# Kernel tuning notes

Hardware: AMD Instinct MI355X
Metric: run time of the kernel (lower is better)

The kernel has to match this reference:

```python
import jax, jax.numpy as jnp
import numpy as np

B, N, L, D, V = 32, 2048, 128, 1024, 32000

def setup_inputs() -> dict:
    key = jax.random.key(0)
    k1, k2, k3 = jax.random.split(key, 3)
    image_features = jax.random.normal(k1, (B, N, D), dtype=jnp.float32)
    token_ids = jax.random.randint(k2, (B, L), 0, V, dtype=jnp.int64)
    emb_table = jax.random.normal(k3, (V, D), dtype=jnp.float32)
    return {"image_features": image_features, "token_ids": token_ids, "emb_table": emb_table}

def reference(image_features, token_ids, emb_table):
    # targets = embeddings(input_ids): [B, L, D]
    targets = emb_table[token_ids]
    # batched pairwise L2 distance (torch.cdist p=2): ||x-y|| via the
    # expanded form ||x||^2 + ||y||^2 - 2<x,y>, clamped for numerical safety.
    x2 = jnp.sum(image_features * image_features, axis=-1)        # [B, N]
    y2 = jnp.sum(targets * targets, axis=-1)                      # [B, L]
    xy = jnp.einsum('bnd,bld->bnl', image_features, targets)      # [B, N, L]
    d2 = x2[:, :, None] + y2[:, None, :] - 2.0 * xy
    costs = jnp.sqrt(jnp.maximum(d2, 0.0))                        # [B, N, L]
    smallest = jnp.min(costs, axis=-1)                            # [B, N]
    return smallest.mean()
```

## Files before the change

kernel.cpp:

```cpp
#include <hip/hip_runtime.h>
#include <cstdint>
#include <cstddef>

#define BATCH 32
#define NROW  2048
#define LTOK  128
#define DDIM  1024

#define BM    128
#define BK    64
#define LDST  72

typedef short s8v  __attribute__((ext_vector_type(8)));
typedef float f4v  __attribute__((ext_vector_type(4)));

__device__ __forceinline__ uint32_t pk2(float lo, float hi) {
    return __builtin_amdgcn_perm(__float_as_uint(hi), __float_as_uint(lo), 0x07060302u);
}

__global__ __launch_bounds__(256)
void prep_y(const int*   __restrict__ tok,
            const float* __restrict__ E,
            uint32_t*    __restrict__ Ybf,
            float*       __restrict__ y2)
{
    const int l = blockIdx.x, b = blockIdx.y;
    const int tid = threadIdx.x;
    const int t = tok[b * LTOK + l];
    const float4 v = ((const float4*)(E + (size_t)t * DDIM))[tid];
    float s = v.x*v.x + v.y*v.y + v.z*v.z + v.w*v.w;
    uint2 p; p.x = pk2(v.x, v.y); p.y = pk2(v.z, v.w);
    ((uint2*)(Ybf + ((size_t)(b * LTOK + l) * DDIM) / 2))[tid] = p;
#pragma unroll
    for (int o = 1; o < 64; o <<= 1) s += __shfl_xor(s, o);
    __shared__ float ws4[4];
    if ((tid & 63) == 0) ws4[tid >> 6] = s;
    __syncthreads();
    if (tid == 0) y2[b * LTOK + l] = ws4[0] + ws4[1] + ws4[2] + ws4[3];
}

__global__ __launch_bounds__(256, 2)
void cdist_min_mean_kernel(const float* __restrict__ X,
                           const short* __restrict__ Ybf,
                           const float* __restrict__ y2g,
                           float* __restrict__ out)
{
    __shared__ __align__(16) short Xs[BM * LDST];
    __shared__ __align__(16) short Ys[LTOK * 64];
    __shared__ float x2s[BM];
    __shared__ float rowmin[BM * 2];
    __shared__ float wsum[4];

    const int tid  = threadIdx.x;
    const int lane = tid & 63;
    const int wid  = tid >> 6;
    const int grp  = tid >> 3;
    const int sub  = tid & 7;

    const int b       = blockIdx.y;
    const int rowBase = blockIdx.x * BM;

    const float* Xg = X + ((size_t)b * NROW + rowBase) * DDIM;

    const float* xp[4];
#pragma unroll
    for (int i = 0; i < 4; ++i)
        xp[i] = Xg + (size_t)(grp + 32 * i) * DDIM + sub * 8;

    const short* yg[4];
#pragma unroll
    for (int it = 0; it < 4; ++it) {
        int c   = it * 256 + tid;
        int row = c >> 3;
        int chs = (c & 7) ^ (row & 7);
        yg[it] = Ybf + (size_t)(b * LTOK + row) * DDIM + chs * 8;
    }

    f4v acc[4][4];
#pragma unroll
    for (int mi = 0; mi < 4; ++mi)
#pragma unroll
        for (int ni = 0; ni < 4; ++ni)
            acc[mi][ni] = (f4v){0.f, 0.f, 0.f, 0.f};

    float xacc[4] = {0.f, 0.f, 0.f, 0.f};

    const int quad = lane >> 4;
    const int l15  = lane & 15;
    const int wm   = wid >> 1;
    const int wn   = wid & 1;

    for (int k0 = 0; k0 < DDIM; k0 += BK) {
        float4 xa[4], xb[4];
#pragma unroll
        for (int i = 0; i < 4; ++i) {
            xa[i] = *(const float4*)(xp[i] + k0);
            xb[i] = *(const float4*)(xp[i] + k0 + 4);
        }
        __syncthreads();

#pragma unroll
        for (int it = 0; it < 4; ++it)
            __builtin_amdgcn_global_load_lds(
                (const __attribute__((address_space(1))) void*)(yg[it] + k0),
                (__attribute__((address_space(3))) void*)&Ys[(it * 256 + (wid << 6)) * 8],
                16, 0, 0);

#pragma unroll
        for (int i = 0; i < 4; ++i) {
            const float4 a = xa[i], c4 = xb[i];
            xacc[i] += a.x*a.x + a.y*a.y + a.z*a.z + a.w*a.w
                     + c4.x*c4.x + c4.y*c4.y + c4.z*c4.z + c4.w*c4.w;
            uint4 p;
            p.x = pk2(a.x, a.y);  p.y = pk2(a.z, a.w);
            p.z = pk2(c4.x, c4.y); p.w = pk2(c4.z, c4.w);
            *(uint4*)&Xs[(grp + 32 * i) * LDST + sub * 8] = p;
        }
        __syncthreads();

#pragma unroll
        for (int ks = 0; ks < BK; ks += 32) {
            s8v af[4], bfr[4];
#pragma unroll
            for (int mi = 0; mi < 4; ++mi)
                af[mi] = *(const s8v*)&Xs[(wm * 64 + mi * 16 + l15) * LDST + ks + quad * 8];
#pragma unroll
            for (int ni = 0; ni < 4; ++ni) {
                int brow = wn * 64 + ni * 16 + l15;
                int ch   = ((ks >> 3) + quad) ^ (brow & 7);
                bfr[ni]  = *(const s8v*)&Ys[brow * 64 + ch * 8];
            }
#pragma unroll
            for (int mi = 0; mi < 4; ++mi)
#pragma unroll
                for (int ni = 0; ni < 4; ++ni)
                    acc[mi][ni] = __builtin_amdgcn_mfma_f32_16x16x32_bf16(
                        af[mi], bfr[ni], acc[mi][ni], 0, 0, 0);
        }
    }

#pragma unroll
    for (int i = 0; i < 4; ++i) {
        float s = xacc[i];
        s += __shfl_xor(s, 1); s += __shfl_xor(s, 2); s += __shfl_xor(s, 4);
        if ((lane & 7) == 0) x2s[grp + 32 * i] = s;
    }
    __syncthreads();

    float y2r[4];
#pragma unroll
    for (int ni = 0; ni < 4; ++ni)
        y2r[ni] = y2g[b * LTOK + wn * 64 + ni * 16 + l15];

#pragma unroll
    for (int mi = 0; mi < 4; ++mi) {
#pragma unroll
        for (int j = 0; j < 4; ++j) {
            float m = y2r[0] - 2.f * acc[mi][0][j];
            m = fminf(m, y2r[1] - 2.f * acc[mi][1][j]);
            m = fminf(m, y2r[2] - 2.f * acc[mi][2][j]);
            m = fminf(m, y2r[3] - 2.f * acc[mi][3][j]);
            m = fminf(m, __shfl_xor(m, 1));
            m = fminf(m, __shfl_xor(m, 2));
            m = fminf(m, __shfl_xor(m, 4));
            m = fminf(m, __shfl_xor(m, 8));
            if (l15 == 0)
                rowmin[(wm * 64 + mi * 16 + quad * 4 + j) * 2 + wn] = m;
        }
    }
    __syncthreads();

    float part = 0.f;
    if (tid < BM) {
        float m = fminf(rowmin[tid * 2], rowmin[tid * 2 + 1]);
        part = sqrtf(fmaxf(x2s[tid] + m, 0.f));
    }
#pragma unroll
    for (int s = 1; s < 64; s <<= 1) part += __shfl_xor(part, s);
    if (lane == 0) wsum[wid] = part;
    __syncthreads();
    if (tid == 0) {
        float tot = (wsum[0] + wsum[1] + wsum[2] + wsum[3])
                  * (1.0f / (float)(BATCH * NROW));
        atomicAdd(out, tot);
    }
}

extern "C" void kernel_launch(void* const* d_in, const int* in_sizes, int n_in,
                              void* d_out, int out_size, void* d_ws, size_t ws_size,
                              hipStream_t stream) {
    const float* X   = (const float*)d_in[0];
    const int*   tok = (const int*)d_in[1];
    const float* E   = (const float*)d_in[2];
    float* out = (float*)d_out;

    uint32_t* Ybf = (uint32_t*)d_ws;
    float*    y2  = (float*)((char*)d_ws + (size_t)BATCH * LTOK * DDIM * 2);

    hipMemsetAsync(out, 0, sizeof(float), stream);

    dim3 pgrid(LTOK, BATCH, 1);
    prep_y<<<pgrid, 256, 0, stream>>>(tok, E, Ybf, y2);

    dim3 grid(NROW / BM, BATCH, 1);
    cdist_min_mean_kernel<<<grid, 256, 0, stream>>>(X, (const short*)Ybf, y2, out);
}
```

Baseline: 440.1 us.

## Drop LDS staging; feed MFMA fragments straight from global with prepacked Y

```diff
diff --git a/kernel.cpp b/kernel.cpp
--- a/kernel.cpp
+++ b/kernel.cpp
@@ -6,13 +6,11 @@
 #define NROW  2048
 #define LTOK  128
 #define DDIM  1024
+#define BM    64
+#define KC    (DDIM / 8)
 
-#define BM    128
-#define BK    64
-#define LDST  72
-
-typedef short s8v  __attribute__((ext_vector_type(8)));
-typedef float f4v  __attribute__((ext_vector_type(4)));
+typedef short s8v __attribute__((ext_vector_type(8)));
+typedef float f4v __attribute__((ext_vector_type(4)));
 
 __device__ __forceinline__ uint32_t pk2(float lo, float hi) {
     return __builtin_amdgcn_perm(__float_as_uint(hi), __float_as_uint(lo), 0x07060302u);
@@ -21,32 +19,30 @@
 __global__ __launch_bounds__(256)
 void prep_y(const int*   __restrict__ tok,
             const float* __restrict__ E,
-            uint32_t*    __restrict__ Ybf,
+            uint32_t*    __restrict__ Ypk,
             float*       __restrict__ y2)
 {
-    const int l = blockIdx.x, b = blockIdx.y;
-    const int tid = threadIdx.x;
-    const int t = tok[b * LTOK + l];
-    const float4 v = ((const float4*)(E + (size_t)t * DDIM))[tid];
+    const int t = blockIdx.x, b = blockIdx.y, tid = threadIdx.x;
+    const int tr = tok[b * LTOK + t];
+    const float4 v = ((const float4*)(E + (size_t)tr * DDIM))[tid];
     float s = v.x*v.x + v.y*v.y + v.z*v.z + v.w*v.w;
+    const int kc = tid >> 1;
     uint2 p; p.x = pk2(v.x, v.y); p.y = pk2(v.z, v.w);
-    ((uint2*)(Ybf + ((size_t)(b * LTOK + l) * DDIM) / 2))[tid] = p;
+    *(uint2*)(Ypk + (((size_t)(b * KC + kc) * LTOK + t) << 2) + ((tid & 1) << 1)) = p;
 #pragma unroll
     for (int o = 1; o < 64; o <<= 1) s += __shfl_xor(s, o);
     __shared__ float ws4[4];
     if ((tid & 63) == 0) ws4[tid >> 6] = s;
     __syncthreads();
-    if (tid == 0) y2[b * LTOK + l] = ws4[0] + ws4[1] + ws4[2] + ws4[3];
+    if (tid == 0) y2[b * LTOK + t] = ws4[0] + ws4[1] + ws4[2] + ws4[3];
 }
 
-__global__ __launch_bounds__(256, 2)
+__global__ __launch_bounds__(256, 4)
 void cdist_min_mean_kernel(const float* __restrict__ X,
-                           const short* __restrict__ Ybf,
+                           const short* __restrict__ Ypk,
                            const float* __restrict__ y2g,
                            float* __restrict__ out)
 {
-    __shared__ __align__(16) short Xs[BM * LDST];
-    __shared__ __align__(16) short Ys[LTOK * 64];
     __shared__ float x2s[BM];
     __shared__ float rowmin[BM * 2];
     __shared__ float wsum[4];
@@ -54,106 +50,88 @@
     const int tid  = threadIdx.x;
     const int lane = tid & 63;
     const int wid  = tid >> 6;
-    const int grp  = tid >> 3;
-    const int sub  = tid & 7;
+    const int l15  = lane & 15;
+    const int quad = lane >> 4;
+    const int wrow = wid >> 1;
+    const int wcol = wid & 1;
 
-    const int b       = blockIdx.y;
-    const int rowBase = blockIdx.x * BM;
+    const int L   = blockIdx.x;
+    const int xcd = L & 7;
+    const int s   = L >> 3;
+    const int b   = (xcd << 2) | (s >> 5);
+    const int rowBase = (s & 31) * BM;
 
-    const float* Xg = X + ((size_t)b * NROW + rowBase) * DDIM;
-
-    const float* xp[4];
+    const float* xp[2];
 #pragma unroll
-    for (int i = 0; i < 4; ++i)
-        xp[i] = Xg + (size_t)(grp + 32 * i) * DDIM + sub * 8;
-
-    const short* yg[4];
+    for (int mi = 0; mi < 2; ++mi) {
+        int row = rowBase + wrow * 32 + mi * 16 + l15;
+        xp[mi] = X + ((size_t)b * NROW + row) * DDIM + quad * 8;
+    }
+    const s8v* ypp[4];
 #pragma unroll
-    for (int it = 0; it < 4; ++it) {
-        int c   = it * 256 + tid;
-        int row = c >> 3;
-        int chs = (c & 7) ^ (row & 7);
-        yg[it] = Ybf + (size_t)(b * LTOK + row) * DDIM + chs * 8;
+    for (int ni = 0; ni < 4; ++ni) {
+        int tcol = wcol * 64 + ni * 16 + l15;
+        ypp[ni] = (const s8v*)Ypk + ((size_t)(b * KC + quad) * LTOK + tcol);
     }
 
-    f4v acc[4][4];
+    f4v acc[2][4];
 #pragma unroll
-    for (int mi = 0; mi < 4; ++mi)
+    for (int mi = 0; mi < 2; ++mi)
 #pragma unroll
         for (int ni = 0; ni < 4; ++ni)
             acc[mi][ni] = (f4v){0.f, 0.f, 0.f, 0.f};
 
-    float xacc[4] = {0.f, 0.f, 0.f, 0.f};
+    float xs2[2] = {0.f, 0.f};
 
-    const int quad = lane >> 4;
-    const int l15  = lane & 15;
-    const int wm   = wid >> 1;
-    const int wn   = wid & 1;
+#pragma unroll 2
+    for (int k0 = 0; k0 < DDIM; k0 += 32) {
+        float4 xa[2], xb[2];
+#pragma unroll
+        for (int mi = 0; mi < 2; ++mi) {
+            xa[mi] = *(const float4*)(xp[mi] + k0);
+            xb[mi] = *(const float4*)(xp[mi] + k0 + 4);
+        }
+        s8v bfr[4];
+        const int yoff = (k0 >> 3) * LTOK;
+#pragma unroll
+        for (int ni = 0; ni < 4; ++ni)
+            bfr[ni] = ypp[ni][yoff];
 
-    for (int k0 = 0; k0 < DDIM; k0 += BK) {
-        float4 xa[4], xb[4];
+        s8v afr[2];
 #pragma unroll
-        for (int i = 0; i < 4; ++i) {
-            xa[i] = *(const float4*)(xp[i] + k0);
-            xb[i] = *(const float4*)(xp[i] + k0 + 4);
+        for (int mi = 0; mi < 2; ++mi) {
+            const float4 a = xa[mi], c = xb[mi];
+            if (wcol == 0)
+                xs2[mi] += a.x*a.x + a.y*a.y + a.z*a.z + a.w*a.w
+                         + c.x*c.x + c.y*c.y + c.z*c.z + c.w*c.w;
+            uint4 p;
+            p.x = pk2(a.x, a.y); p.y = pk2(a.z, a.w);
+            p.z = pk2(c.x, c.y); p.w = pk2(c.z, c.w);
+            afr[mi] = *(s8v*)&p;
         }
-        __syncthreads();
-
 #pragma unroll
-        for (int it = 0; it < 4; ++it)
-            __builtin_amdgcn_global_load_lds(
-                (const __attribute__((address_space(1))) void*)(yg[it] + k0),
-                (__attribute__((address_space(3))) void*)&Ys[(it * 256 + (wid << 6)) * 8],
-                16, 0, 0);
-
+        for (int mi = 0; mi < 2; ++mi)
 #pragma unroll
-        for (int i = 0; i < 4; ++i) {
-            const float4 a = xa[i], c4 = xb[i];
-            xacc[i] += a.x*a.x + a.y*a.y + a.z*a.z + a.w*a.w
-                     + c4.x*c4.x + c4.y*c4.y + c4.z*c4.z + c4.w*c4.w;
-            uint4 p;
-            p.x = pk2(a.x, a.y);  p.y = pk2(a.z, a.w);
-            p.z = pk2(c4.x, c4.y); p.w = pk2(c4.z, c4.w);
-            *(uint4*)&Xs[(grp + 32 * i) * LDST + sub * 8] = p;
-        }
-        __syncthreads();
-
-#pragma unroll
-        for (int ks = 0; ks < BK; ks += 32) {
-            s8v af[4], bfr[4];
-#pragma unroll
-            for (int mi = 0; mi < 4; ++mi)
-                af[mi] = *(const s8v*)&Xs[(wm * 64 + mi * 16 + l15) * LDST + ks + quad * 8];
-#pragma unroll
-            for (int ni = 0; ni < 4; ++ni) {
-                int brow = wn * 64 + ni * 16 + l15;
-                int ch   = ((ks >> 3) + quad) ^ (brow & 7);
-                bfr[ni]  = *(const s8v*)&Ys[brow * 64 + ch * 8];
-            }
-#pragma unroll
-            for (int mi = 0; mi < 4; ++mi)
-#pragma unroll
-                for (int ni = 0; ni < 4; ++ni)
-                    acc[mi][ni] = __builtin_amdgcn_mfma_f32_16x16x32_bf16(
-                        af[mi], bfr[ni], acc[mi][ni], 0, 0, 0);
-        }
+            for (int ni = 0; ni < 4; ++ni)
+                acc[mi][ni] = __builtin_amdgcn_mfma_f32_16x16x32_bf16(
+                    afr[mi], bfr[ni], acc[mi][ni], 0, 0, 0);
     }
 
 #pragma unroll
-    for (int i = 0; i < 4; ++i) {
-        float s = xacc[i];
-        s += __shfl_xor(s, 1); s += __shfl_xor(s, 2); s += __shfl_xor(s, 4);
-        if ((lane & 7) == 0) x2s[grp + 32 * i] = s;
+    for (int mi = 0; mi < 2; ++mi) {
+        float v = xs2[mi];
+        v += __shfl_xor(v, 16);
+        v += __shfl_xor(v, 32);
+        if (wcol == 0 && quad == 0) x2s[wrow * 32 + mi * 16 + l15] = v;
     }
-    __syncthreads();
 
     float y2r[4];
 #pragma unroll
     for (int ni = 0; ni < 4; ++ni)
-        y2r[ni] = y2g[b * LTOK + wn * 64 + ni * 16 + l15];
+        y2r[ni] = y2g[b * LTOK + wcol * 64 + ni * 16 + l15];
 
 #pragma unroll
-    for (int mi = 0; mi < 4; ++mi) {
+    for (int mi = 0; mi < 2; ++mi) {
 #pragma unroll
         for (int j = 0; j < 4; ++j) {
             float m = y2r[0] - 2.f * acc[mi][0][j];
@@ -165,7 +143,7 @@
             m = fminf(m, __shfl_xor(m, 4));
             m = fminf(m, __shfl_xor(m, 8));
             if (l15 == 0)
-                rowmin[(wm * 64 + mi * 16 + quad * 4 + j) * 2 + wn] = m;
+                rowmin[(wrow * 32 + mi * 16 + quad * 4 + j) * 2 + wcol] = m;
         }
     }
     __syncthreads();
@@ -176,7 +154,7 @@
         part = sqrtf(fmaxf(x2s[tid] + m, 0.f));
     }
 #pragma unroll
-    for (int s = 1; s < 64; s <<= 1) part += __shfl_xor(part, s);
+    for (int o = 1; o < 64; o <<= 1) part += __shfl_xor(part, o);
     if (lane == 0) wsum[wid] = part;
     __syncthreads();
     if (tid == 0) {
@@ -194,14 +172,14 @@
     const float* E   = (const float*)d_in[2];
     float* out = (float*)d_out;
 
-    uint32_t* Ybf = (uint32_t*)d_ws;
-    float*    y2  = (float*)((char*)d_ws + (size_t)BATCH * LTOK * DDIM * 2);
+    uint32_t* Ypk = (uint32_t*)d_ws;
+    float*    y2  = (float*)((char*)d_ws + (size_t)BATCH * KC * LTOK * 16);
 
     hipMemsetAsync(out, 0, sizeof(float), stream);
 
     dim3 pgrid(LTOK, BATCH, 1);
-    prep_y<<<pgrid, 256, 0, stream>>>(tok, E, Ybf, y2);
+    prep_y<<<pgrid, 256, 0, stream>>>(tok, E, Ypk, y2);
 
-    dim3 grid(NROW / BM, BATCH, 1);
-    cdist_min_mean_kernel<<<grid, 256, 0, stream>>>(X, (const short*)Ybf, y2, out);
+    cdist_min_mean_kernel<<<dim3(1024, 1, 1), 256, 0, stream>>>(
+        X, (const short*)Ypk, y2, out);
 }
```

New measurement: 447.0 us. No clear change (+1.6%).
